# Optimization experiments

Measured on AMD Instinct MI355X. Metric: run time of the kernel, lower is better.

## Reference

```python
import jax, jax.numpy as jnp
import numpy as np
from jax import lax

GAMMA = 0.01618
NEG_SLOPE = 0.01  # torch leaky_relu default


def setup_inputs() -> dict:
    key = jax.random.key(0)
    k1, k2 = jax.random.split(key)
    N, D_in, D_out = 8192, 1024, 4096
    X = jax.random.normal(k1, (N, D_in), dtype=jnp.float32)
    # xavier_uniform_ for Linear weight (fan_in=D_in, fan_out=D_out)
    bound = float(np.sqrt(6.0 / (D_in + D_out)))
    W = jax.random.uniform(k2, (D_out, D_in), dtype=jnp.float32, minval=-bound, maxval=bound)
    b = jnp.zeros((D_out,), dtype=jnp.float32)
    return {"X": X, "W": W, "b": b, "k": 10}


def reference(X, W, b, k):
    # fc1 + leaky_relu: [N, D_out]
    h = jax.nn.leaky_relu(X @ W.T + b, negative_slope=NEG_SLOPE)
    D_out = h.shape[1]

    def step(phi, row):
        s = row * phi                                   # gate by inhibition mask
        vals, idx = lax.top_k(s, k)                     # per-row top-k
        scattered = jnp.zeros_like(s).at[idx].set(vals)
        # 'binary' mask_type: >0 -> 1, everything else -> 0
        binary = (scattered > 0.0).astype(s.dtype)
        # phi[phi<1] += gamma; phi[phi>=1] = 1; phi *= (1 - binary)
        phi2 = jnp.minimum(jnp.where(phi < 1.0, phi + GAMMA, phi), 1.0)
        phi2 = phi2 * (1.0 - binary)
        return phi2, binary

    phi0 = jnp.ones((D_out,), dtype=h.dtype)
    _, out = lax.scan(step, phi0, h)  # sequential recurrence over batch rows
    return out
```

## Files before the change

kernel.cpp:

```cpp
#include <hip/hip_runtime.h>
#include <cstdint>
#include <cstddef>

typedef unsigned long long u64;
typedef unsigned int u32;

#define NROWS 8192
#define DIN   1024
#define DOUT  4096
#define GAMMA 0.01618f
#define NC    640
#define RQ    2048
#define BATCH 8

typedef _Float16 f16x8 __attribute__((ext_vector_type(8)));
typedef float    f32x4 __attribute__((ext_vector_type(4)));

__device__ __forceinline__ u32 mono_key(float f) {
    u32 u = __float_as_uint(f);
    return (u & 0x80000000u) ? ~u : (u | 0x80000000u);
}
__device__ __forceinline__ u32 unmono_key(u32 u) {
    return (u & 0x80000000u) ? (u ^ 0x80000000u) : ~u;
}

__device__ __forceinline__ u64 wave_max64(u64 x) {
#pragma unroll
    for (int off = 32; off >= 1; off >>= 1) {
        u32 lo = (u32)x, hi = (u32)(x >> 32);
        u32 olo = __shfl_xor(lo, off, 64);
        u32 ohi = __shfl_xor(hi, off, 64);
        u64 o = ((u64)ohi << 32) | olo;
        if (o > x) x = o;
    }
    return x;
}
__device__ __forceinline__ u64 shfl_u64(u64 x, int src) {
    u32 lo = __shfl((u32)x, src, 64);
    u32 hi = __shfl((u32)(x >> 32), src, 64);
    return ((u64)hi << 32) | lo;
}

__device__ __forceinline__ void gl16(const void* g, void* l) {
    __builtin_amdgcn_global_load_lds(
        (const __attribute__((address_space(1))) unsigned int*)g,
        (__attribute__((address_space(3))) unsigned int*)l, 16, 0, 0);
}

__global__ __launch_bounds__(256)
void split_kernel(const float* __restrict__ X, const float* __restrict__ W,
                  _Float16* __restrict__ X1, _Float16* __restrict__ X2,
                  _Float16* __restrict__ W1, _Float16* __restrict__ W2) {
    int t = blockIdx.x * 256 + threadIdx.x;
    const int NXG = (NROWS * DIN) / 8;
    const int NWG = (DOUT * DIN) / 8;
    if (t >= NXG + NWG) return;
    const float* src; _Float16* d1; _Float16* d2; int row, g8;
    if (t < NXG) { src = X; d1 = X1; d2 = X2; row = t >> 7; g8 = t & 127; }
    else { int u = t - NXG; src = W; d1 = W1; d2 = W2; row = u >> 7; g8 = u & 127; }
    const int kb = g8 >> 2, gp = g8 & 3;
    const int g  = gp ^ ((row >> 1) & 3);
    const int kbase = kb * 32 + g * 4;
    const float* p = src + (size_t)row * DIN + kbase;
    float4 lo = *(const float4*)p;
    float4 hi = *(const float4*)(p + 16);
    float xs[8] = {lo.x, lo.y, lo.z, lo.w, hi.x, hi.y, hi.z, hi.w};
    f16x8 v1, v2;
#pragma unroll
    for (int e = 0; e < 8; ++e) {
        float x  = xs[e];
        float x1 = (float)(_Float16)x;
        if (fabsf(x1) < 6.103515625e-05f) x1 = 0.0f;
        v1[e] = (_Float16)x1;
        v2[e] = (_Float16)((x - x1) * 2048.0f);
    }
    size_t o = (size_t)row * DIN + (size_t)g8 * 8;
    *(f16x8*)(d1 + o) = v1;
    *(f16x8*)(d2 + o) = v2;
}

__global__ __launch_bounds__(256, 2)
void gemm_f16x2_mfma(const _Float16* __restrict__ X1, const _Float16* __restrict__ X2,
                     const _Float16* __restrict__ W1, const _Float16* __restrict__ W2,
                     const float* __restrict__ bias, float* __restrict__ H) {
    __shared__ _Float16 SM[12288];
    const int tid  = threadIdx.x;
    const int lane = tid & 63, w = tid >> 6;
    const int wm = w >> 1, wn = w & 1;
    const int m0 = blockIdx.y * 128, n0 = blockIdx.x * 64;

    const char* gp6[6];
    unsigned loff[6];
#pragma unroll
    for (int q = 0; q < 6; ++q) {
        int G = tid + q * 256;
        const char* base; int rowg, c;
        if (G < 1024) {
            int s = G >> 9, rem = G & 511; rowg = m0 + (rem >> 2); c = rem & 3;
            base = (const char*)(s ? X2 : X1);
        } else {
            int Gb = G - 1024;
            int s = Gb >> 8, rem = Gb & 255; rowg = n0 + (rem >> 2); c = rem & 3;
            base = (const char*)(s ? W2 : W1);
        }
        gp6[q]  = base + (size_t)rowg * (DIN * 2) + (size_t)c * 16;
        loff[q] = (unsigned)((w * 64 + q * 256) * 16);
    }

    f32x4 accHH[4][2], accM[4][2];
    double hd[4][2][4];
    const f32x4 z4 = {0.f, 0.f, 0.f, 0.f};
#pragma unroll
    for (int i = 0; i < 4; ++i)
#pragma unroll
        for (int j = 0; j < 2; ++j) {
            accHH[i][j] = z4; accM[i][j] = z4;
#pragma unroll
            for (int r = 0; r < 4; ++r) hd[i][j][r] = 0.0;
        }

    const int fr  = lane & 15;
    const int gsw = (lane >> 4) ^ ((lane >> 1) & 3);
    const int aoff = fr * 32 + gsw * 8;
    const int boff = 8192 + (wn * 32 + fr) * 32 + gsw * 8;

    for (int ks = 0; ks < 32; ++ks) {
#pragma unroll
        for (int q = 0; q < 6; ++q)
            gl16(gp6[q] + (size_t)ks * 64, (char*)SM + loff[q]);
        __syncthreads();

        f16x8 a1[4], a2[4], b1[2], b2[2];
#pragma unroll
        for (int i = 0; i < 4; ++i) {
            const _Float16* pa = SM + (wm * 64 + i * 16) * 32 + aoff;
            a1[i] = *(const f16x8*)pa;
            a2[i] = *(const f16x8*)(pa + 4096);
        }
#pragma unroll
        for (int j = 0; j < 2; ++j) {
            const _Float16* pb = SM + boff + j * 16 * 32;
            b1[j] = *(const f16x8*)pb;
            b2[j] = *(const f16x8*)(pb + 2048);
        }
#pragma unroll
        for (int i = 0; i < 4; ++i)
#pragma unroll
            for (int j = 0; j < 2; ++j) {
                accHH[i][j] = __builtin_amdgcn_mfma_f32_16x16x32_f16(a1[i], b1[j], accHH[i][j], 0, 0, 0);
                accM[i][j]  = __builtin_amdgcn_mfma_f32_16x16x32_f16(a1[i], b2[j], accM[i][j],  0, 0, 0);
                accM[i][j]  = __builtin_amdgcn_mfma_f32_16x16x32_f16(a2[i], b1[j], accM[i][j],  0, 0, 0);
            }
        if (ks & 1) {
#pragma unroll
            for (int i = 0; i < 4; ++i)
#pragma unroll
                for (int j = 0; j < 2; ++j) {
#pragma unroll
                    for (int r = 0; r < 4; ++r) hd[i][j][r] += (double)accHH[i][j][r];
                    accHH[i][j] = z4;
                }
        }
        __syncthreads();
    }

    const int fq = lane >> 4;
#pragma unroll
    for (int i = 0; i < 4; ++i)
#pragma unroll
        for (int j = 0; j < 2; ++j) {
            const int col = n0 + wn * 32 + j * 16 + fr;
            const double bb = (double)bias[col];
#pragma unroll
            for (int r = 0; r < 4; ++r) {
                const int row = m0 + wm * 64 + i * 16 + fq * 4 + r;
                double v = hd[i][j][r] + (double)accM[i][j][r] * (1.0 / 2048.0) + bb;
                float h = (float)v;
                h = (h >= 0.0f) ? h : 0.01f * h;
                H[(size_t)row * DOUT + col] = h;
            }
        }
}

__global__ __launch_bounds__(256)
void topk640_kernel(float* __restrict__ H) {
    __shared__ u32 skey[DOUT];
    __shared__ int hist[DOUT];
    __shared__ u64 scand[1024];
    __shared__ int seg[256];
    __shared__ int s_b, s_cnt;
    const int row = blockIdx.x;
    const int tid = threadIdx.x;
    float* hrow = H + (size_t)row * DOUT;

#pragma unroll
    for (int c = 0; c < 4; c++) {
        int j = c * 1024 + tid * 4;
        float4 v = *(const float4*)(hrow + j);
        skey[j + 0] = mono_key(v.x); skey[j + 1] = mono_key(v.y);
        skey[j + 2] = mono_key(v.z); skey[j + 3] = mono_key(v.w);
    }
#pragma unroll
    for (int c = 0; c < 16; c++) hist[c * 256 + tid] = 0;
    if (tid == 0) s_cnt = 0;
    __syncthreads();
#pragma unroll
    for (int c = 0; c < 4; c++) {
        int j = c * 1024 + tid * 4;
        atomicAdd(&hist[skey[j + 0] >> 20], 1);
        atomicAdd(&hist[skey[j + 1] >> 20], 1);
        atomicAdd(&hist[skey[j + 2] >> 20], 1);
        atomicAdd(&hist[skey[j + 3] >> 20], 1);
    }
    __syncthreads();
    {
        int ssum = 0;
#pragma unroll
        for (int i = 0; i < 16; i++) ssum += hist[tid * 16 + i];
        seg[tid] = ssum;
    }
    __syncthreads();
    if (tid == 0) {
        int cum = 0, ts;
        for (ts = 255; ts >= 0; ts--) {
            if (cum + seg[ts] >= NC) break;
            cum += seg[ts];
        }
        int b = 0;
        if (ts >= 0) {
            int bin;
            for (bin = ts * 16 + 15; bin >= ts * 16; bin--) {
                cum += hist[bin];
                if (cum >= NC) break;
            }
            b = (bin < ts * 16) ? ts * 16 : bin;
        }
        s_b = b;
    }
    __syncthreads();
    const int b = s_b;
#pragma unroll
    for (int c = 0; c < 4; c++) {
        int jb = c * 1024 + tid * 4;
#pragma unroll
        for (int q = 0; q < 4; q++) {
            int j = jb + q;
            u32 k = skey[j];
            if ((int)(k >> 20) >= b) {
                int pos = atomicAdd(&s_cnt, 1);
                if (pos < 1024)
                    scand[pos] = ((u64)k << 32) | (u32)(0xFFFFu - (u32)j);
            }
        }
    }
    __syncthreads();
    int C = s_cnt; if (C > 1024) C = 1024;
    for (int j = C + tid; j < 1024; j += 256) scand[j] = 0;
    for (int size = 2; size <= 1024; size <<= 1)
        for (int stride = size >> 1; stride > 0; stride >>= 1) {
            __syncthreads();
#pragma unroll 2
            for (int i = tid; i < 512; i += 256) {
                int pos = 2 * i - (i & (stride - 1));
                u64 a = scand[pos], bb = scand[pos + stride];
                bool up = (pos & size) == 0;
                if ((a < bb) == up) { scand[pos] = bb; scand[pos + stride] = a; }
            }
        }
    __syncthreads();
    u64* cand = (u64*)hrow;
    for (int j = tid; j < NC; j += 256) cand[j] = scand[j];
}

__device__ __forceinline__ void row_top10(
    int m, u64 c, u64 k64, const u64* __restrict__ crow,
    const int* last_sel, float tbl_r, int lane, u64 lmask_lt,
    bool& sel, u32& mid)
{
    const int id = 0xFFFF - (int)(c & 0xFFFFu);
    int t = m - last_sel[id] - 1; if (t > 63) t = 63;
    const bool unsup = (t >= 62);
    const u64 mu = __ballot(unsup);
    const float phi = __shfl(tbl_r, t);
    const float v = __uint_as_float(unmono_key((u32)(c >> 32)));
    const float s = v * phi;
    const u64 skey = ((u64)mono_key(s) << 32) | (c & 0xFFFFu);
    const int nu = __popcll(mu);
    const int prefix = __popcll(mu & lmask_lt);

    bool resolved = false, win = false;
    if (nu >= 10) {
        u64 um = mu;
#pragma unroll
        for (int q = 0; q < 9; q++) um &= um - 1;
        const int lane10 = __ffsll((long long)um) - 1;
        const u64 key10 = shfl_u64(skey, lane10);
        const u64 beat = __ballot(skey > key10) & ~mu;
        u64 theta;
        if (beat == 0ull) {
            win = unsup && (prefix < 10);
            theta = key10;
        } else {
            int myExtra = 0, myrank = 64;
            u64 bm = beat;
            while (bm) {
                const int l = __ffsll((long long)bm) - 1;
                bm &= bm - 1;
                const u64 kb = shfl_u64(skey, l);
                const u64 g = __ballot(skey > kb);
                if (lane == l) myrank = __popcll(g);
                myExtra += (kb > skey) ? 1 : 0;
            }
            const bool isbeat = (beat >> lane) & 1ull;
            const int rank = unsup ? (prefix + myExtra) : (isbeat ? myrank : 64);
            win = rank < 10;
            const u64 r9 = __ballot(rank == 9);
            const int l9 = __ffsll((long long)r9) - 1;
            theta = shfl_u64(skey, l9);
        }
        resolved = ((u32)(theta >> 32) > 0x80000000u) && (theta > k64);
    }

    if (resolved) {
        sel = win; mid = (u32)id;
        return;
    }
    u64 tt[10];
    u64 key = skey, key2 = 0;
#pragma unroll 1
    for (int it = 0; it < 10; it++) {
        if (it > 0) {
            u64 ck = crow[it * 64 + lane];
            u32 hbits = unmono_key((u32)(ck >> 32));
            int id2 = 0xFFFF - (int)(ck & 0xFFFFu);
            int t2 = m - last_sel[id2] - 1; if (t2 > 63) t2 = 63;
            float s2 = __uint_as_float(hbits) * __shfl(tbl_r, t2);
            key = ((u64)mono_key(s2) << 32) | (ck & 0xFFFFu);
            key2 = 0;
#pragma unroll
            for (int rr = 0; rr < 10; rr++) if (lane == rr) key2 = tt[rr];
        }
#pragma unroll
        for (int rr = 0; rr < 10; rr++) {
            u64 mx = (key > key2) ? key : key2;
            u64 wm = wave_max64(mx);
            if (key == wm)  key = 0;
            if (key2 == wm) key2 = 0;
            tt[rr] = wm;
        }
        if (it == 9) break;
        u32 thr = (u32)(tt[9] >> 32);
        u32 headhi = (u32)(crow[(it + 1) * 64] >> 32);
        if (thr > 0x80000000u && thr > headhi) break;
    }
    u64 wk = 0;
#pragma unroll
    for (int rr = 0; rr < 10; rr++) if (lane == rr) wk = tt[rr];
    sel = (lane < 10) && ((u32)(wk >> 32) > 0x80000000u);
    mid = (u32)(0xFFFF - (int)(wk & 0xFFFFu));
}

__global__ __launch_bounds__(512)
void scan_kernel(const u64* __restrict__ cand, float* __restrict__ out) {
    __shared__ int last_sel[DOUT];
    __shared__ u32 specw[BATCH][16];
    __shared__ u64 chunk0[BATCH][64];
    __shared__ u64 k64s[BATCH];
    __shared__ u32 staleF[BATCH];
    const int tid  = threadIdx.x;
    const int lane = tid & 63;
    const int w    = tid >> 6;

    for (int j = tid; j < DOUT; j += 512) last_sel[j] = -100000;

    float tbl_r = 0.0f;
    {
        float p = 0.0f;
        for (int i = 0; i < 64; i++) {
            if (i == lane) tbl_r = p;
            p = fminf(p + GAMMA, 1.0f);
        }
    }
    const u64 lmask_lt = (lane == 0) ? 0ull : ((1ull << lane) - 1ull);
    __syncthreads();

    u64 cpre = cand[(size_t)w * RQ + lane];
    u64 kpre = cand[(size_t)w * RQ + 64];

    for (int m0 = 0; m0 < NROWS; m0 += BATCH) {
        const int m = m0 + w;
        const u64 c  = cpre;
        const u64 kk = kpre;
        int mp = m + BATCH; if (mp >= NROWS) mp = w;
        cpre = cand[(size_t)mp * RQ + lane];
        kpre = cand[(size_t)mp * RQ + 64];

        bool sel; u32 mid;
        row_top10(m, c, kk, cand + (size_t)m * RQ, last_sel, tbl_r, lane,
                  lmask_lt, sel, mid);

        if (lane < 16) specw[w][lane] = 0xFFFFFFFFu;
        const u64 smask = __ballot(sel);
        const int slot = __popcll(smask & lmask_lt);
        if (sel) specw[w][slot] = mid;
        chunk0[w][lane] = c;
        if (lane == 0) k64s[w] = kk;
        __syncthreads();

        u32 my[10];
#pragma unroll
        for (int q = 0; q < 10; q++) my[q] = specw[w][q];
        bool hit = false;
#pragma unroll
        for (int pass = 0; pass < 2; pass++) {
            const int e = lane + pass * 64;
            if (e < BATCH * 10) {
                const int i = e / 10, j = e - i * 10;
                if (i < w) {
                    const u32 eid = specw[i][j];
                    if (eid != 0xFFFFFFFFu) {
#pragma unroll
                        for (int q = 0; q < 10; q++) hit |= (eid == my[q]);
                    }
                }
            }
        }
        const u32 st = __ballot(hit) ? 1u : 0u;
        if (lane == 0) staleF[w] = st;
        __syncthreads();

        int firstStale = BATCH;
#pragma unroll
        for (int i = BATCH - 1; i >= 0; i--) if (staleF[i]) firstStale = i;

        if (w < firstStale && sel) {
            out[(size_t)m * DOUT + mid] = 1.0f;
            last_sel[mid] = m;
        }
        __syncthreads();

        if (w == 0 && firstStale < BATCH) {
            for (int i = firstStale; i < BATCH; i++) {
                const int mi = m0 + i;
                const u32 sid = (lane < 10) ? specw[i][lane] : 0xFFFFFFFFu;
                const bool has = (sid != 0xFFFFFFFFu);
                const int ls2 = has ? last_sel[sid] : -100000;
                const u64 stale = __ballot(has && (ls2 >= m0));
                if (stale == 0ull) {
                    if (has) {
                        out[(size_t)mi * DOUT + sid] = 1.0f;
                        last_sel[sid] = mi;
                    }
                } else {
                    bool s2; u32 mid2;
                    row_top10(mi, chunk0[i][lane], k64s[i],
                              cand + (size_t)mi * RQ, last_sel, tbl_r, lane,
                              lmask_lt, s2, mid2);
                    if (s2) {
                        out[(size_t)mi * DOUT + mid2] = 1.0f;
                        last_sel[mid2] = mi;
                    }
                }
            }
        }
        __syncthreads();
    }
}

extern "C" void kernel_launch(void* const* d_in, const int* in_sizes, int n_in,
                              void* d_out, int out_size, void* d_ws, size_t ws_size,
                              hipStream_t stream) {
    const float* X  = (const float*)d_in[0];
    const float* Wt = (const float*)d_in[1];
    const float* b  = (const float*)d_in[2];
    float* out = (float*)d_out;
    float* H   = (float*)d_ws;
    (void)in_sizes; (void)n_in; (void)out_size; (void)ws_size;

    char* ob = (char*)d_out;
    _Float16* X1 = (_Float16*)(ob);
    _Float16* X2 = (_Float16*)(ob + (size_t)16 * 1024 * 1024);
    _Float16* W1 = (_Float16*)(ob + (size_t)32 * 1024 * 1024);
    _Float16* W2 = (_Float16*)(ob + (size_t)40 * 1024 * 1024);

    split_kernel<<<dim3(6144), 256, 0, stream>>>(X, Wt, X1, X2, W1, W2);
    gemm_f16x2_mfma<<<dim3(DOUT / 64, NROWS / 128), 256, 0, stream>>>(X1, X2, W1, W2, b, H);
    topk640_kernel<<<dim3(NROWS), 256, 0, stream>>>(H);
    hipMemsetAsync(d_out, 0, (size_t)NROWS * DOUT * sizeof(float), stream);
    scan_kernel<<<dim3(1), 512, 0, stream>>>((const u64*)H, out);
}
```

Baseline: 2.574 ms.

## Double speculative scan batch and recompute stale rows in parallel rounds

```diff
diff --git a/kernel.cpp b/kernel.cpp
--- a/kernel.cpp
+++ b/kernel.cpp
@@ -11,7 +11,7 @@
 #define GAMMA 0.01618f
 #define NC    640
 #define RQ    2048
-#define BATCH 8
+#define BATCH 16
 
 typedef _Float16 f16x8 __attribute__((ext_vector_type(8)));
 typedef float    f32x4 __attribute__((ext_vector_type(4)));
@@ -360,7 +360,7 @@
     mid = (u32)(0xFFFF - (int)(wk & 0xFFFFu));
 }
 
-__global__ __launch_bounds__(512)
+__global__ __launch_bounds__(1024)
 void scan_kernel(const u64* __restrict__ cand, float* __restrict__ out) {
     __shared__ int last_sel[DOUT];
     __shared__ u32 specw[BATCH][16];
@@ -371,7 +371,7 @@
     const int lane = tid & 63;
     const int w    = tid >> 6;
 
-    for (int j = tid; j < DOUT; j += 512) last_sel[j] = -100000;
+    for (int j = tid; j < DOUT; j += 1024) last_sel[j] = -100000;
 
     float tbl_r = 0.0f;
     {
@@ -407,63 +407,63 @@
         if (lane == 0) k64s[w] = kk;
         __syncthreads();
 
-        u32 my[10];
-#pragma unroll
-        for (int q = 0; q < 10; q++) my[q] = specw[w][q];
-        bool hit = false;
-#pragma unroll
-        for (int pass = 0; pass < 2; pass++) {
-            const int e = lane + pass * 64;
-            if (e < BATCH * 10) {
-                const int i = e / 10, j = e - i * 10;
-                if (i < w) {
-                    const u32 eid = specw[i][j];
-                    if (eid != 0xFFFFFFFFu) {
-#pragma unroll
-                        for (int q = 0; q < 10; q++) hit |= (eid == my[q]);
+        int fs = 0;
+        while (true) {
+            u32 my[10];
+#pragma unroll
+            for (int q = 0; q < 10; q++) my[q] = specw[w][q];
+            bool hit = false;
+#pragma unroll
+            for (int pass = 0; pass * 64 < BATCH * 10; pass++) {
+                const int e = lane + pass * 64;
+                if (e < BATCH * 10) {
+                    const int i = e / 10, j = e - i * 10;
+                    if (i >= fs && i < w) {
+                        const u32 eid = specw[i][j];
+                        if (eid != 0xFFFFFFFFu) {
+#pragma unroll
+                            for (int q = 0; q < 10; q++) hit |= (eid == my[q]);
+                        }
                     }
                 }
             }
-        }
-        const u32 st = __ballot(hit) ? 1u : 0u;
-        if (lane == 0) staleF[w] = st;
-        __syncthreads();
-
-        int firstStale = BATCH;
-#pragma unroll
-        for (int i = BATCH - 1; i >= 0; i--) if (staleF[i]) firstStale = i;
-
-        if (w < firstStale && sel) {
-            out[(size_t)m * DOUT + mid] = 1.0f;
-            last_sel[mid] = m;
-        }
-        __syncthreads();
-
-        if (w == 0 && firstStale < BATCH) {
-            for (int i = firstStale; i < BATCH; i++) {
-                const int mi = m0 + i;
-                const u32 sid = (lane < 10) ? specw[i][lane] : 0xFFFFFFFFu;
+            const u32 st = __ballot(hit) ? 1u : 0u;
+            if (lane == 0) staleF[w] = st;
+            __syncthreads();
+
+            int nfs = BATCH;
+#pragma unroll
+            for (int i = BATCH - 1; i >= 0; i--)
+                if (i >= fs && staleF[i]) nfs = i;
+
+            if (w >= fs && w < nfs) {
+                const u32 sid = (lane < 10) ? specw[w][lane] : 0xFFFFFFFFu;
+                if (sid != 0xFFFFFFFFu) {
+                    out[(size_t)m * DOUT + sid] = 1.0f;
+                    last_sel[sid] = m;
+                }
+            }
+            __syncthreads();
+            fs = nfs;
+            if (fs >= BATCH) break;
+
+            if (w >= fs) {
+                const u32 sid = (lane < 10) ? specw[w][lane] : 0xFFFFFFFFu;
                 const bool has = (sid != 0xFFFFFFFFu);
                 const int ls2 = has ? last_sel[sid] : -100000;
-                const u64 stale = __ballot(has && (ls2 >= m0));
-                if (stale == 0ull) {
-                    if (has) {
-                        out[(size_t)mi * DOUT + sid] = 1.0f;
-                        last_sel[sid] = mi;
-                    }
-                } else {
+                if (__ballot(has && (ls2 >= m0))) {
                     bool s2; u32 mid2;
-                    row_top10(mi, chunk0[i][lane], k64s[i],
-                              cand + (size_t)mi * RQ, last_sel, tbl_r, lane,
+                    row_top10(m, chunk0[w][lane], k64s[w],
+                              cand + (size_t)m * RQ, last_sel, tbl_r, lane,
                               lmask_lt, s2, mid2);
-                    if (s2) {
-                        out[(size_t)mi * DOUT + mid2] = 1.0f;
-                        last_sel[mid2] = mi;
-                    }
+                    if (lane < 16) specw[w][lane] = 0xFFFFFFFFu;
+                    const u64 sm2 = __ballot(s2);
+                    const int sl2 = __popcll(sm2 & lmask_lt);
+                    if (s2) specw[w][sl2] = mid2;
                 }
             }
-        }
-        __syncthreads();
+            __syncthreads();
+        }
     }
 }
 
@@ -487,5 +487,5 @@
     gemm_f16x2_mfma<<<dim3(DOUT / 64, NROWS / 128), 256, 0, stream>>>(X1, X2, W1, W2, b, H);
     topk640_kernel<<<dim3(NROWS), 256, 0, stream>>>(H);
     hipMemsetAsync(d_out, 0, (size_t)NROWS * DOUT * sizeof(float), stream);
-    scan_kernel<<<dim3(1), 512, 0, stream>>>((const u64*)H, out);
-}
+    scan_kernel<<<dim3(1), 1024, 0, stream>>>((const u64*)H, out);
+}
```

After: 3.754 ms. 45.8% more time.

## Fuse split, GEMM, top-k and scan into one persistent kernel with flags

Applied to the files above, without the earlier changes.

```diff
diff --git a/kernel.cpp b/kernel.cpp
--- a/kernel.cpp
+++ b/kernel.cpp
@@ -12,9 +12,20 @@
 #define NC    640
 #define RQ    2048
 #define BATCH 8
+#define NWK   255
+#define GQ_SPAN 4351u
+#define TQ_SPAN 8447u
 
 typedef _Float16 f16x8 __attribute__((ext_vector_type(8)));
 typedef float    f32x4 __attribute__((ext_vector_type(4)));
+
+__device__ u32 g_blk = 0;
+__device__ u32 g_gq  = 0;
+__device__ u32 g_tq  = 0;
+__device__ u32 g_chunk[64] = {};
+__device__ u32 g_rowReady[NROWS] = {};
+
+#define SCOPE __HIP_MEMORY_SCOPE_AGENT
 
 __device__ __forceinline__ u32 mono_key(float f) {
     u32 u = __float_as_uint(f);
@@ -41,31 +52,8 @@
     return ((u64)hi << 32) | lo;
 }
 
-__device__ __forceinline__ void gl16(const void* g, void* l) {
-    __builtin_amdgcn_global_load_lds(
-        (const __attribute__((address_space(1))) unsigned int*)g,
-        (__attribute__((address_space(3))) unsigned int*)l, 16, 0, 0);
-}
-
-__global__ __launch_bounds__(256)
-void split_kernel(const float* __restrict__ X, const float* __restrict__ W,
-                  _Float16* __restrict__ X1, _Float16* __restrict__ X2,
-                  _Float16* __restrict__ W1, _Float16* __restrict__ W2) {
-    int t = blockIdx.x * 256 + threadIdx.x;
-    const int NXG = (NROWS * DIN) / 8;
-    const int NWG = (DOUT * DIN) / 8;
-    if (t >= NXG + NWG) return;
-    const float* src; _Float16* d1; _Float16* d2; int row, g8;
-    if (t < NXG) { src = X; d1 = X1; d2 = X2; row = t >> 7; g8 = t & 127; }
-    else { int u = t - NXG; src = W; d1 = W1; d2 = W2; row = u >> 7; g8 = u & 127; }
-    const int kb = g8 >> 2, gp = g8 & 3;
-    const int g  = gp ^ ((row >> 1) & 3);
-    const int kbase = kb * 32 + g * 4;
-    const float* p = src + (size_t)row * DIN + kbase;
-    float4 lo = *(const float4*)p;
-    float4 hi = *(const float4*)(p + 16);
+__device__ __forceinline__ void split8(float4 lo, float4 hi, f16x8& v1, f16x8& v2) {
     float xs[8] = {lo.x, lo.y, lo.z, lo.w, hi.x, hi.y, hi.z, hi.w};
-    f16x8 v1, v2;
 #pragma unroll
     for (int e = 0; e < 8; ++e) {
         float x  = xs[e];
@@ -74,146 +62,140 @@
         v1[e] = (_Float16)x1;
         v2[e] = (_Float16)((x - x1) * 2048.0f);
     }
-    size_t o = (size_t)row * DIN + (size_t)g8 * 8;
-    *(f16x8*)(d1 + o) = v1;
-    *(f16x8*)(d2 + o) = v2;
-}
-
-__global__ __launch_bounds__(256, 2)
-void gemm_f16x2_mfma(const _Float16* __restrict__ X1, const _Float16* __restrict__ X2,
-                     const _Float16* __restrict__ W1, const _Float16* __restrict__ W2,
-                     const float* __restrict__ bias, float* __restrict__ H) {
-    __shared__ _Float16 SM[12288];
-    const int tid  = threadIdx.x;
+}
+
+__device__ void gemm_tile(u32 t, const float* __restrict__ X, const float* __restrict__ Wt,
+                          const float* __restrict__ bias, float* __restrict__ H,
+                          char* dsm, int tid, u32 k) {
+    _Float16* SMf = (_Float16*)dsm;
     const int lane = tid & 63, w = tid >> 6;
-    const int wm = w >> 1, wn = w & 1;
-    const int m0 = blockIdx.y * 128, n0 = blockIdx.x * 64;
-
-    const char* gp6[6];
-    unsigned loff[6];
-#pragma unroll
-    for (int q = 0; q < 6; ++q) {
-        int G = tid + q * 256;
-        const char* base; int rowg, c;
-        if (G < 1024) {
-            int s = G >> 9, rem = G & 511; rowg = m0 + (rem >> 2); c = rem & 3;
-            base = (const char*)(s ? X2 : X1);
-        } else {
-            int Gb = G - 1024;
-            int s = Gb >> 8, rem = Gb & 255; rowg = n0 + (rem >> 2); c = rem & 3;
-            base = (const char*)(s ? W2 : W1);
-        }
-        gp6[q]  = base + (size_t)rowg * (DIN * 2) + (size_t)c * 16;
-        loff[q] = (unsigned)((w * 64 + q * 256) * 16);
-    }
-
-    f32x4 accHH[4][2], accM[4][2];
-    double hd[4][2][4];
+    const int wm = w >> 2, wn = w & 3;
+    const int by = (int)(t >> 6), bx = (int)(t & 63);
+    const int m0 = by * 128, n0 = bx * 64;
+
+    f32x4 accHH[4], accM[4];
+    double hd[4][4];
     const f32x4 z4 = {0.f, 0.f, 0.f, 0.f};
 #pragma unroll
-    for (int i = 0; i < 4; ++i)
-#pragma unroll
-        for (int j = 0; j < 2; ++j) {
-            accHH[i][j] = z4; accM[i][j] = z4;
-#pragma unroll
-            for (int r = 0; r < 4; ++r) hd[i][j][r] = 0.0;
-        }
-
-    const int fr  = lane & 15;
+    for (int i = 0; i < 4; ++i) {
+        accHH[i] = z4; accM[i] = z4;
+#pragma unroll
+        for (int r = 0; r < 4; ++r) hd[i][r] = 0.0;
+    }
+
+    const int fr  = lane & 15, fq = lane >> 4;
     const int gsw = (lane >> 4) ^ ((lane >> 1) & 3);
     const int aoff = fr * 32 + gsw * 8;
-    const int boff = 8192 + (wn * 32 + fr) * 32 + gsw * 8;
+    const int boff = 8192 + (wn * 16 + fr) * 32 + gsw * 8;
+
+    const int ar = tid >> 2, agp = tid & 3;
+    const int ag = agp ^ ((ar >> 1) & 3);
+    const int br = (tid & 255) >> 2, bgp = tid & 3;
+    const int bg = bgp ^ ((br >> 1) & 3);
+    const float* pax = X  + (size_t)(m0 + ar) * DIN + ag * 4;
+    const float* pbw = Wt + (size_t)(n0 + br) * DIN + bg * 4;
+    _Float16* da1 = SMf + ar * 32 + agp * 8;
+    _Float16* da2 = da1 + 4096;
+    _Float16* db1 = SMf + 8192 + br * 32 + bgp * 8;
+    _Float16* db2 = db1 + 2048;
 
     for (int ks = 0; ks < 32; ++ks) {
-#pragma unroll
-        for (int q = 0; q < 6; ++q)
-            gl16(gp6[q] + (size_t)ks * 64, (char*)SM + loff[q]);
-        __syncthreads();
-
-        f16x8 a1[4], a2[4], b1[2], b2[2];
+        {
+            float4 lo = *(const float4*)(pax + ks * 32);
+            float4 hi = *(const float4*)(pax + ks * 32 + 16);
+            f16x8 v1, v2; split8(lo, hi, v1, v2);
+            *(f16x8*)da1 = v1; *(f16x8*)da2 = v2;
+        }
+        if (tid < 256) {
+            float4 lo = *(const float4*)(pbw + ks * 32);
+            float4 hi = *(const float4*)(pbw + ks * 32 + 16);
+            f16x8 v1, v2; split8(lo, hi, v1, v2);
+            *(f16x8*)db1 = v1; *(f16x8*)db2 = v2;
+        }
+        __syncthreads();
+
+        f16x8 a1[4], a2[4], b1, b2;
 #pragma unroll
         for (int i = 0; i < 4; ++i) {
-            const _Float16* pa = SM + (wm * 64 + i * 16) * 32 + aoff;
+            const _Float16* pa = SMf + (wm * 64 + i * 16) * 32 + aoff;
             a1[i] = *(const f16x8*)pa;
             a2[i] = *(const f16x8*)(pa + 4096);
         }
-#pragma unroll
-        for (int j = 0; j < 2; ++j) {
-            const _Float16* pb = SM + boff + j * 16 * 32;
-            b1[j] = *(const f16x8*)pb;
-            b2[j] = *(const f16x8*)(pb + 2048);
-        }
-#pragma unroll
-        for (int i = 0; i < 4; ++i)
-#pragma unroll
-            for (int j = 0; j < 2; ++j) {
-                accHH[i][j] = __builtin_amdgcn_mfma_f32_16x16x32_f16(a1[i], b1[j], accHH[i][j], 0, 0, 0);
-                accM[i][j]  = __builtin_amdgcn_mfma_f32_16x16x32_f16(a1[i], b2[j], accM[i][j],  0, 0, 0);
-                accM[i][j]  = __builtin_amdgcn_mfma_f32_16x16x32_f16(a2[i], b1[j], accM[i][j],  0, 0, 0);
-            }
+        b1 = *(const f16x8*)(SMf + boff);
+        b2 = *(const f16x8*)(SMf + boff + 2048);
+#pragma unroll
+        for (int i = 0; i < 4; ++i) {
+            accHH[i] = __builtin_amdgcn_mfma_f32_16x16x32_f16(a1[i], b1, accHH[i], 0, 0, 0);
+            accM[i]  = __builtin_amdgcn_mfma_f32_16x16x32_f16(a1[i], b2, accM[i],  0, 0, 0);
+            accM[i]  = __builtin_amdgcn_mfma_f32_16x16x32_f16(a2[i], b1, accM[i],  0, 0, 0);
+        }
         if (ks & 1) {
 #pragma unroll
-            for (int i = 0; i < 4; ++i)
-#pragma unroll
-                for (int j = 0; j < 2; ++j) {
-#pragma unroll
-                    for (int r = 0; r < 4; ++r) hd[i][j][r] += (double)accHH[i][j][r];
-                    accHH[i][j] = z4;
-                }
-        }
-        __syncthreads();
-    }
-
-    const int fq = lane >> 4;
-#pragma unroll
-    for (int i = 0; i < 4; ++i)
-#pragma unroll
-        for (int j = 0; j < 2; ++j) {
-            const int col = n0 + wn * 32 + j * 16 + fr;
-            const double bb = (double)bias[col];
-#pragma unroll
-            for (int r = 0; r < 4; ++r) {
-                const int row = m0 + wm * 64 + i * 16 + fq * 4 + r;
-                double v = hd[i][j][r] + (double)accM[i][j][r] * (1.0 / 2048.0) + bb;
-                float h = (float)v;
-                h = (h >= 0.0f) ? h : 0.01f * h;
-                H[(size_t)row * DOUT + col] = h;
-            }
-        }
-}
-
-__global__ __launch_bounds__(256)
-void topk640_kernel(float* __restrict__ H) {
-    __shared__ u32 skey[DOUT];
-    __shared__ int hist[DOUT];
-    __shared__ u64 scand[1024];
-    __shared__ int seg[256];
-    __shared__ int s_b, s_cnt;
-    const int row = blockIdx.x;
-    const int tid = threadIdx.x;
-    float* hrow = H + (size_t)row * DOUT;
-
-#pragma unroll
-    for (int c = 0; c < 4; c++) {
-        int j = c * 1024 + tid * 4;
+            for (int i = 0; i < 4; ++i) {
+#pragma unroll
+                for (int r = 0; r < 4; ++r) hd[i][r] += (double)accHH[i][r];
+                accHH[i] = z4;
+            }
+        }
+        __syncthreads();
+    }
+
+    const int col = n0 + wn * 16 + fr;
+    const double bb = (double)bias[col];
+#pragma unroll
+    for (int i = 0; i < 4; ++i) {
+#pragma unroll
+        for (int r = 0; r < 4; ++r) {
+            const int row = m0 + wm * 64 + i * 16 + fq * 4 + r;
+            double v = hd[i][r] + (double)accM[i][r] * (1.0 / 2048.0) + bb;
+            float h = (float)v;
+            h = (h >= 0.0f) ? h : 0.01f * h;
+            H[(size_t)row * DOUT + col] = h;
+        }
+    }
+    __syncthreads();
+    if (tid == 0)
+        __hip_atomic_fetch_add(&g_chunk[by], 1u, __ATOMIC_RELEASE, SCOPE);
+}
+
+__device__ void topk_row(u32 r, float* __restrict__ H, float* __restrict__ out,
+                         char* dsm, int tid, u32 k) {
+    u32* skey  = (u32*)dsm;
+    int* hist  = (int*)(dsm + 16384);
+    u64* scand = (u64*)(dsm + 32768);
+    int* seg   = (int*)(dsm + 40960);
+    int* s_b   = (int*)(dsm + 41984);
+    int* s_cnt = s_b + 1;
+
+    if (tid == 0) {
+        while (__hip_atomic_load(&g_chunk[r >> 7], __ATOMIC_RELAXED, SCOPE) < (k + 1u) * 64u)
+            __builtin_amdgcn_s_sleep(8);
+    }
+    __syncthreads();
+    __builtin_amdgcn_fence(__ATOMIC_ACQUIRE, "agent");
+
+    float* hrow = H + (size_t)r * DOUT;
+#pragma unroll
+    for (int c = 0; c < 2; c++) {
+        int j = c * 2048 + tid * 4;
         float4 v = *(const float4*)(hrow + j);
         skey[j + 0] = mono_key(v.x); skey[j + 1] = mono_key(v.y);
         skey[j + 2] = mono_key(v.z); skey[j + 3] = mono_key(v.w);
     }
 #pragma unroll
-    for (int c = 0; c < 16; c++) hist[c * 256 + tid] = 0;
-    if (tid == 0) s_cnt = 0;
-    __syncthreads();
-#pragma unroll
-    for (int c = 0; c < 4; c++) {
-        int j = c * 1024 + tid * 4;
+    for (int c = 0; c < 8; c++) hist[c * 512 + tid] = 0;
+    if (tid == 0) *s_cnt = 0;
+    __syncthreads();
+#pragma unroll
+    for (int c = 0; c < 2; c++) {
+        int j = c * 2048 + tid * 4;
         atomicAdd(&hist[skey[j + 0] >> 20], 1);
         atomicAdd(&hist[skey[j + 1] >> 20], 1);
         atomicAdd(&hist[skey[j + 2] >> 20], 1);
         atomicAdd(&hist[skey[j + 3] >> 20], 1);
     }
     __syncthreads();
-    {
+    if (tid < 256) {
         int ssum = 0;
 #pragma unroll
         for (int i = 0; i < 16; i++) ssum += hist[tid * 16 + i];
@@ -235,32 +217,32 @@
             }
             b = (bin < ts * 16) ? ts * 16 : bin;
         }
-        s_b = b;
-    }
-    __syncthreads();
-    const int b = s_b;
-#pragma unroll
-    for (int c = 0; c < 4; c++) {
-        int jb = c * 1024 + tid * 4;
+        *s_b = b;
+    }
+    __syncthreads();
+    const int b = *s_b;
+#pragma unroll
+    for (int c = 0; c < 2; c++) {
+        int jb = c * 2048 + tid * 4;
 #pragma unroll
         for (int q = 0; q < 4; q++) {
             int j = jb + q;
-            u32 k = skey[j];
-            if ((int)(k >> 20) >= b) {
-                int pos = atomicAdd(&s_cnt, 1);
+            u32 kk = skey[j];
+            if ((int)(kk >> 20) >= b) {
+                int pos = atomicAdd(s_cnt, 1);
                 if (pos < 1024)
-                    scand[pos] = ((u64)k << 32) | (u32)(0xFFFFu - (u32)j);
-            }
-        }
-    }
-    __syncthreads();
-    int C = s_cnt; if (C > 1024) C = 1024;
-    for (int j = C + tid; j < 1024; j += 256) scand[j] = 0;
+                    scand[pos] = ((u64)kk << 32) | (u32)(0xFFFFu - (u32)j);
+            }
+        }
+    }
+    __syncthreads();
+    int C = *s_cnt; if (C > 1024) C = 1024;
+    for (int j = C + tid; j < 1024; j += 512) scand[j] = 0;
     for (int size = 2; size <= 1024; size <<= 1)
         for (int stride = size >> 1; stride > 0; stride >>= 1) {
             __syncthreads();
-#pragma unroll 2
-            for (int i = tid; i < 512; i += 256) {
+            {
+                int i = tid;
                 int pos = 2 * i - (i & (stride - 1));
                 u64 a = scand[pos], bb = scand[pos + stride];
                 bool up = (pos & size) == 0;
@@ -269,7 +251,15 @@
         }
     __syncthreads();
     u64* cand = (u64*)hrow;
-    for (int j = tid; j < NC; j += 256) cand[j] = scand[j];
+    for (int j = tid; j < NC; j += 512) cand[j] = scand[j];
+    {
+        float4 z = {0.f, 0.f, 0.f, 0.f};
+        float4* po = (float4*)(out + (size_t)r * DOUT);
+        po[tid] = z; po[tid + 512] = z;
+    }
+    __syncthreads();
+    if (tid == 0)
+        __hip_atomic_store(&g_rowReady[r], k + 1u, __ATOMIC_RELEASE, SCOPE);
 }
 
 __device__ __forceinline__ void row_top10(
@@ -360,14 +350,18 @@
     mid = (u32)(0xFFFF - (int)(wk & 0xFFFFu));
 }
 
-__global__ __launch_bounds__(512)
-void scan_kernel(const u64* __restrict__ cand, float* __restrict__ out) {
-    __shared__ int last_sel[DOUT];
-    __shared__ u32 specw[BATCH][16];
-    __shared__ u64 chunk0[BATCH][64];
-    __shared__ u64 k64s[BATCH];
-    __shared__ u32 staleF[BATCH];
-    const int tid  = threadIdx.x;
+__device__ __forceinline__ void wait_row(int r, u32 k) {
+    while (__hip_atomic_load(&g_rowReady[r], __ATOMIC_RELAXED, SCOPE) < k + 1u) {}
+    __builtin_amdgcn_fence(__ATOMIC_ACQUIRE, "agent");
+}
+
+__device__ void scan_role(const u64* __restrict__ cand, float* __restrict__ out,
+                          char* dsm, int tid, u32 kEpoch) {
+    int* last_sel      = (int*)dsm;
+    u32 (*specw)[16]   = (u32(*)[16])(dsm + 16384);
+    u64 (*chunk0)[64]  = (u64(*)[64])(dsm + 16896);
+    u64* k64s          = (u64*)(dsm + 20992);
+    u32* staleF        = (u32*)(dsm + 21056);
     const int lane = tid & 63;
     const int w    = tid >> 6;
 
@@ -384,6 +378,7 @@
     const u64 lmask_lt = (lane == 0) ? 0ull : ((1ull << lane) - 1ull);
     __syncthreads();
 
+    wait_row(w, kEpoch);
     u64 cpre = cand[(size_t)w * RQ + lane];
     u64 kpre = cand[(size_t)w * RQ + 64];
 
@@ -392,6 +387,7 @@
         const u64 c  = cpre;
         const u64 kk = kpre;
         int mp = m + BATCH; if (mp >= NROWS) mp = w;
+        wait_row(mp, kEpoch);
         cpre = cand[(size_t)mp * RQ + lane];
         kpre = cand[(size_t)mp * RQ + 64];
 
@@ -467,6 +463,43 @@
     }
 }
 
+__global__ __launch_bounds__(512, 2)
+void mega_kernel(const float* __restrict__ X, const float* __restrict__ Wt,
+                 const float* __restrict__ bias, float* __restrict__ H,
+                 float* __restrict__ out) {
+    extern __shared__ char dsm[];
+    __shared__ u32 sh_k, sh_t;
+    const int tid = threadIdx.x;
+
+    if (tid == 0)
+        sh_k = __hip_atomic_fetch_add(&g_blk, 1u, __ATOMIC_RELAXED, SCOPE) >> 8;
+    __syncthreads();
+    const u32 k = sh_k;
+
+    if (blockIdx.x == NWK) {
+        scan_role((const u64*)H, out, dsm, tid, k);
+        return;
+    }
+    for (;;) {
+        __syncthreads();
+        if (tid == 0)
+            sh_t = __hip_atomic_fetch_add(&g_gq, 1u, __ATOMIC_RELAXED, SCOPE) - k * GQ_SPAN;
+        __syncthreads();
+        u32 t = sh_t;
+        if (t >= 4096u) break;
+        gemm_tile(t, X, Wt, bias, H, dsm, tid, k);
+    }
+    for (;;) {
+        __syncthreads();
+        if (tid == 0)
+            sh_t = __hip_atomic_fetch_add(&g_tq, 1u, __ATOMIC_RELAXED, SCOPE) - k * TQ_SPAN;
+        __syncthreads();
+        u32 r = sh_t;
+        if (r >= 8192u) break;
+        topk_row(r, H, out, dsm, tid, k);
+    }
+}
+
 extern "C" void kernel_launch(void* const* d_in, const int* in_sizes, int n_in,
                               void* d_out, int out_size, void* d_ws, size_t ws_size,
                               hipStream_t stream) {
@@ -477,15 +510,5 @@
     float* H   = (float*)d_ws;
     (void)in_sizes; (void)n_in; (void)out_size; (void)ws_size;
 
-    char* ob = (char*)d_out;
-    _Float16* X1 = (_Float16*)(ob);
-    _Float16* X2 = (_Float16*)(ob + (size_t)16 * 1024 * 1024);
-    _Float16* W1 = (_Float16*)(ob + (size_t)32 * 1024 * 1024);
-    _Float16* W2 = (_Float16*)(ob + (size_t)40 * 1024 * 1024);
-
-    split_kernel<<<dim3(6144), 256, 0, stream>>>(X, Wt, X1, X2, W1, W2);
-    gemm_f16x2_mfma<<<dim3(DOUT / 64, NROWS / 128), 256, 0, stream>>>(X1, X2, W1, W2, b, H);
-    topk640_kernel<<<dim3(NROWS), 256, 0, stream>>>(H);
-    hipMemsetAsync(d_out, 0, (size_t)NROWS * DOUT * sizeof(float), stream);
-    scan_kernel<<<dim3(1), 512, 0, stream>>>((const u64*)H, out);
-}
+    mega_kernel<<<dim3(NWK + 1), dim3(512), 43008, stream>>>(X, Wt, b, H, out);
+}
```

Result: slower. 4.581 ms (+78.0%).

## Fuse top-k prefilter and sequential scan into one persistent producer-consumer kernel

Applied to the files above, without the earlier changes.

```diff
diff --git a/kernel.cpp b/kernel.cpp
--- a/kernel.cpp
+++ b/kernel.cpp
@@ -12,9 +12,16 @@
 #define NC    640
 #define RQ    2048
 #define BATCH 8
+#define TQ_SPAN 8447u
 
 typedef _Float16 f16x8 __attribute__((ext_vector_type(8)));
 typedef float    f32x4 __attribute__((ext_vector_type(4)));
+
+__device__ u32 g_blk = 0;
+__device__ u32 g_tq  = 0;
+__device__ u32 g_rowReady[NROWS] = {};
+
+#define SCOPE __HIP_MEMORY_SCOPE_AGENT
 
 __device__ __forceinline__ u32 mono_key(float f) {
     u32 u = __float_as_uint(f);
@@ -182,38 +189,37 @@
         }
 }
 
-__global__ __launch_bounds__(256)
-void topk640_kernel(float* __restrict__ H) {
-    __shared__ u32 skey[DOUT];
-    __shared__ int hist[DOUT];
-    __shared__ u64 scand[1024];
-    __shared__ int seg[256];
-    __shared__ int s_b, s_cnt;
-    const int row = blockIdx.x;
-    const int tid = threadIdx.x;
-    float* hrow = H + (size_t)row * DOUT;
-
-#pragma unroll
-    for (int c = 0; c < 4; c++) {
-        int j = c * 1024 + tid * 4;
+__device__ void topk_row(u32 r, float* __restrict__ H, float* __restrict__ out,
+                         char* dsm, int tid, u32 k) {
+    u32* skey  = (u32*)dsm;
+    int* hist  = (int*)(dsm + 16384);
+    u64* scand = (u64*)(dsm + 32768);
+    int* seg   = (int*)(dsm + 40960);
+    int* s_b   = (int*)(dsm + 41984);
+    int* s_cnt = s_b + 1;
+
+    float* hrow = H + (size_t)r * DOUT;
+#pragma unroll
+    for (int c = 0; c < 2; c++) {
+        int j = c * 2048 + tid * 4;
         float4 v = *(const float4*)(hrow + j);
         skey[j + 0] = mono_key(v.x); skey[j + 1] = mono_key(v.y);
         skey[j + 2] = mono_key(v.z); skey[j + 3] = mono_key(v.w);
     }
 #pragma unroll
-    for (int c = 0; c < 16; c++) hist[c * 256 + tid] = 0;
-    if (tid == 0) s_cnt = 0;
-    __syncthreads();
-#pragma unroll
-    for (int c = 0; c < 4; c++) {
-        int j = c * 1024 + tid * 4;
+    for (int c = 0; c < 8; c++) hist[c * 512 + tid] = 0;
+    if (tid == 0) *s_cnt = 0;
+    __syncthreads();
+#pragma unroll
+    for (int c = 0; c < 2; c++) {
+        int j = c * 2048 + tid * 4;
         atomicAdd(&hist[skey[j + 0] >> 20], 1);
         atomicAdd(&hist[skey[j + 1] >> 20], 1);
         atomicAdd(&hist[skey[j + 2] >> 20], 1);
         atomicAdd(&hist[skey[j + 3] >> 20], 1);
     }
     __syncthreads();
-    {
+    if (tid < 256) {
         int ssum = 0;
 #pragma unroll
         for (int i = 0; i < 16; i++) ssum += hist[tid * 16 + i];
@@ -235,32 +241,32 @@
             }
             b = (bin < ts * 16) ? ts * 16 : bin;
         }
-        s_b = b;
-    }
-    __syncthreads();
-    const int b = s_b;
-#pragma unroll
-    for (int c = 0; c < 4; c++) {
-        int jb = c * 1024 + tid * 4;
+        *s_b = b;
+    }
+    __syncthreads();
+    const int b = *s_b;
+#pragma unroll
+    for (int c = 0; c < 2; c++) {
+        int jb = c * 2048 + tid * 4;
 #pragma unroll
         for (int q = 0; q < 4; q++) {
             int j = jb + q;
-            u32 k = skey[j];
-            if ((int)(k >> 20) >= b) {
-                int pos = atomicAdd(&s_cnt, 1);
+            u32 kk = skey[j];
+            if ((int)(kk >> 20) >= b) {
+                int pos = atomicAdd(s_cnt, 1);
                 if (pos < 1024)
-                    scand[pos] = ((u64)k << 32) | (u32)(0xFFFFu - (u32)j);
-            }
-        }
-    }
-    __syncthreads();
-    int C = s_cnt; if (C > 1024) C = 1024;
-    for (int j = C + tid; j < 1024; j += 256) scand[j] = 0;
+                    scand[pos] = ((u64)kk << 32) | (u32)(0xFFFFu - (u32)j);
+            }
+        }
+    }
+    __syncthreads();
+    int C = *s_cnt; if (C > 1024) C = 1024;
+    for (int j = C + tid; j < 1024; j += 512) scand[j] = 0;
     for (int size = 2; size <= 1024; size <<= 1)
         for (int stride = size >> 1; stride > 0; stride >>= 1) {
             __syncthreads();
-#pragma unroll 2
-            for (int i = tid; i < 512; i += 256) {
+            {
+                int i = tid;
                 int pos = 2 * i - (i & (stride - 1));
                 u64 a = scand[pos], bb = scand[pos + stride];
                 bool up = (pos & size) == 0;
@@ -269,7 +275,15 @@
         }
     __syncthreads();
     u64* cand = (u64*)hrow;
-    for (int j = tid; j < NC; j += 256) cand[j] = scand[j];
+    for (int j = tid; j < NC; j += 512) cand[j] = scand[j];
+    {
+        float4 z = {0.f, 0.f, 0.f, 0.f};
+        float4* po = (float4*)(out + (size_t)r * DOUT);
+        po[tid] = z; po[tid + 512] = z;
+    }
+    __syncthreads();
+    if (tid == 0)
+        __hip_atomic_store(&g_rowReady[r], k + 1u, __ATOMIC_RELEASE, SCOPE);
 }
 
 __device__ __forceinline__ void row_top10(
@@ -360,14 +374,18 @@
     mid = (u32)(0xFFFF - (int)(wk & 0xFFFFu));
 }
 
-__global__ __launch_bounds__(512)
-void scan_kernel(const u64* __restrict__ cand, float* __restrict__ out) {
-    __shared__ int last_sel[DOUT];
-    __shared__ u32 specw[BATCH][16];
-    __shared__ u64 chunk0[BATCH][64];
-    __shared__ u64 k64s[BATCH];
-    __shared__ u32 staleF[BATCH];
-    const int tid  = threadIdx.x;
+__device__ __forceinline__ void wait_row(int r, u32 k) {
+    while (__hip_atomic_load(&g_rowReady[r], __ATOMIC_RELAXED, SCOPE) < k + 1u) {}
+    __builtin_amdgcn_fence(__ATOMIC_ACQUIRE, "agent");
+}
+
+__device__ void scan_role(const u64* __restrict__ cand, float* __restrict__ out,
+                          char* dsm, int tid, u32 kEpoch) {
+    int* last_sel      = (int*)dsm;
+    u32 (*specw)[16]   = (u32(*)[16])(dsm + 16384);
+    u64 (*chunk0)[64]  = (u64(*)[64])(dsm + 16896);
+    u64* k64s          = (u64*)(dsm + 20992);
+    u32* staleF        = (u32*)(dsm + 21056);
     const int lane = tid & 63;
     const int w    = tid >> 6;
 
@@ -384,6 +402,7 @@
     const u64 lmask_lt = (lane == 0) ? 0ull : ((1ull << lane) - 1ull);
     __syncthreads();
 
+    wait_row(w, kEpoch);
     u64 cpre = cand[(size_t)w * RQ + lane];
     u64 kpre = cand[(size_t)w * RQ + 64];
 
@@ -392,6 +411,7 @@
         const u64 c  = cpre;
         const u64 kk = kpre;
         int mp = m + BATCH; if (mp >= NROWS) mp = w;
+        wait_row(mp, kEpoch);
         cpre = cand[(size_t)mp * RQ + lane];
         kpre = cand[(size_t)mp * RQ + 64];
 
@@ -467,6 +487,32 @@
     }
 }
 
+__global__ __launch_bounds__(512, 2)
+void topk_scan_kernel(float* __restrict__ H, float* __restrict__ out) {
+    extern __shared__ char dsm[];
+    __shared__ u32 sh_k, sh_t;
+    const int tid = threadIdx.x;
+
+    if (tid == 0)
+        sh_k = __hip_atomic_fetch_add(&g_blk, 1u, __ATOMIC_RELAXED, SCOPE) >> 8;
+    __syncthreads();
+    const u32 k = sh_k;
+
+    if (blockIdx.x == 0) {
+        scan_role((const u64*)H, out, dsm, tid, k);
+        return;
+    }
+    for (;;) {
+        __syncthreads();
+        if (tid == 0)
+            sh_t = __hip_atomic_fetch_add(&g_tq, 1u, __ATOMIC_RELAXED, SCOPE) - k * TQ_SPAN;
+        __syncthreads();
+        u32 r = sh_t;
+        if (r >= 8192u) break;
+        topk_row(r, H, out, dsm, tid, k);
+    }
+}
+
 extern "C" void kernel_launch(void* const* d_in, const int* in_sizes, int n_in,
                               void* d_out, int out_size, void* d_ws, size_t ws_size,
                               hipStream_t stream) {
@@ -485,7 +531,5 @@
 
     split_kernel<<<dim3(6144), 256, 0, stream>>>(X, Wt, X1, X2, W1, W2);
     gemm_f16x2_mfma<<<dim3(DOUT / 64, NROWS / 128), 256, 0, stream>>>(X1, X2, W1, W2, b, H);
-    topk640_kernel<<<dim3(NROWS), 256, 0, stream>>>(H);
-    hipMemsetAsync(d_out, 0, (size_t)NROWS * DOUT * sizeof(float), stream);
-    scan_kernel<<<dim3(1), 512, 0, stream>>>((const u64*)H, out);
-}
+    topk_scan_kernel<<<dim3(256), dim3(512), 43008, stream>>>(H, out);
+}
```

Result: slower. 2.671 ms (+3.8%).
